# Kernel tuning notes

Hardware: AMD Instinct MI355X
Metric: run time of the kernel (lower is better)

The kernel has to match this reference:

```python
import jax, jax.numpy as jnp
import numpy as np

N = 768; H = 12; SQK = 16; SV = 16; PQK = 4; PV = 8; C = 384; PD = 128
EPS = 1e-8


def setup_inputs() -> dict:
    key = jax.random.key(0)
    ks = jax.random.split(key, 12)
    rn = lambda k, s, sc=1.0: jax.random.normal(k, s, jnp.float32) * sc
    return {
        'inputs_1d': rn(ks[0], (N, C)),
        'inputs_2d': rn(ks[1], (N, N, PD)),
        'mask': jnp.ones((N, 1), jnp.float32),
        'rotation': rn(ks[2], (9, N)),
        'translation': rn(ks[3], (3, N)),
        'wq': rn(ks[4], (C, H * SQK), C ** -0.5), 'bq': jnp.zeros((H * SQK,), jnp.float32),
        'wkv': rn(ks[5], (C, H * (SQK + SV)), C ** -0.5), 'bkv': jnp.zeros((H * (SQK + SV),), jnp.float32),
        'wqp': rn(ks[6], (C, H * 3 * PQK), C ** -0.5), 'bqp': jnp.zeros((H * 3 * PQK,), jnp.float32),
        'wkvp': rn(ks[7], (C, H * 3 * (PQK + PV)), C ** -0.5), 'bkvp': jnp.zeros((H * 3 * (PQK + PV),), jnp.float32),
        'tpw': jnp.ones((H,), jnp.float32),
        'w2d': rn(ks[8], (PD, H), PD ** -0.5), 'b2d': jnp.zeros((H,), jnp.float32),
        'wout': rn(ks[9], (H * (SV + 4 * PV + PD), C), 0.02), 'bout': jnp.zeros((C,), jnp.float32),
    }


def reference(inputs_1d, inputs_2d, mask, rotation, translation, wq, bq, wkv, bkv,
              wqp, bqp, wkvp, bkvp, tpw, w2d, b2d, wout, bout):
    n = inputs_1d.shape[0]
    R = rotation[:, :, None]
    T = translation[:, :, None]

    def apply_pt(x, y, z):  # global = R @ local + t, per residue
        return (R[0] * x + R[1] * y + R[2] * z + T[0],
                R[3] * x + R[4] * y + R[5] * z + T[1],
                R[6] * x + R[7] * y + R[8] * z + T[2])

    # scalar q/k/v
    qs = (inputs_1d @ wq + bq).reshape(n, H, SQK)
    kvs = (inputs_1d @ wkv + bkv).reshape(n, H, SQK + SV)
    ks_, vs = kvs[..., :SQK], kvs[..., SQK:]

    # point q and k/v in global frame
    qx, qy, qz = jnp.split(inputs_1d @ wqp + bqp, 3, axis=-1)
    q_pt = jnp.stack(apply_pt(qx, qy, qz), 0).reshape(3, n, H, PQK).transpose(0, 2, 1, 3)  # [3,H,N,PQK]
    kx, ky, kz = jnp.split(inputs_1d @ wkvp + bkvp, 3, axis=-1)
    kv_pt = jnp.stack(apply_pt(kx, ky, kz), 0).reshape(3, n, H, PQK + PV).transpose(0, 2, 1, 3)
    k_pt, v_pt = kv_pt[..., :PQK], kv_pt[..., PQK:]  # [3,H,N,PQK], [3,H,N,PV]

    # point attention term
    pw = jnp.sqrt(1.0 / (3 * 18)) * jax.nn.softplus(tpw)  # [H]
    dist2 = jnp.sum(jnp.square(q_pt[:, :, :, None, :] - k_pt[:, :, None, :, :]), axis=0)  # [H,N,N,PQK]
    attn_qk_point = -0.5 * jnp.sum(pw[:, None, None, None] * dist2, axis=-1)  # [H,N,N]

    # scalar attention term
    sw = jnp.sqrt(1.0 / (3 * 16))
    attn_qk_scalar = jnp.einsum('ihc,jhc->hij', sw * qs, ks_)

    # pair bias
    att2d = jnp.sqrt(1.0 / 3) * jnp.transpose(inputs_2d @ w2d + b2d, (2, 0, 1))  # [H,N,N]

    mask2d = mask * mask.T  # [N,N]
    logits = attn_qk_scalar + attn_qk_point + att2d - 50.0 * (1.0 - mask2d)
    attn = jax.nn.softmax(logits, axis=-1)  # [H,N,N]

    # weighted values
    res_scalar = jnp.einsum('hij,jhc->ihc', attn, vs).reshape(n, H * SV)
    res_pt = jnp.einsum('hij,dhjp->dihp', attn, v_pt).reshape(3, n, H * PV)

    # invert rigid: local = R^T @ (global - t)
    gx, gy, gz = res_pt[0] - T[0], res_pt[1] - T[1], res_pt[2] - T[2]
    lx = R[0] * gx + R[3] * gy + R[6] * gz
    ly = R[1] * gx + R[4] * gy + R[7] * gz
    lz = R[2] * gx + R[5] * gy + R[8] * gz
    dist = jnp.sqrt(EPS + lx * lx + ly * ly + lz * lz)

    res2d = jnp.einsum('hij,ijc->ihc', attn, inputs_2d).reshape(n, H * PD)

    feat = jnp.concatenate([res_scalar, lx, ly, lz, dist, res2d], axis=-1)  # [N, 2112]
    return feat @ wout + bout
```

## Files before the change

kernel.cpp:

```cpp
#include <hip/hip_runtime.h>
#include <cstdint>
#include <cstddef>


#define N_RES 768
#define NHEAD 12
#define NN (768*768)

__device__ __forceinline__ float softplusf_(float x) {
  return (x > 20.f) ? x : log1pf(__expf(x));
}

__global__ __launch_bounds__(256) void pack_b_kernel(
    const float* __restrict__ wq, const float* __restrict__ wkv,
    const float* __restrict__ wqp, const float* __restrict__ wkvp,
    float* __restrict__ B_all)
{
  int idx4 = blockIdx.x * 256 + threadIdx.x;
  int k = idx4 / 288;
  int n = (idx4 - k*288) * 4;
  float4 v;
  if (n < 192)       v = *(const float4*)(wq   + (size_t)k*192 + n);
  else if (n < 576)  v = *(const float4*)(wkv  + (size_t)k*384 + (n-192));
  else if (n < 720)  v = *(const float4*)(wqp  + (size_t)k*144 + (n-576));
  else               v = *(const float4*)(wkvp + (size_t)k*432 + (n-720));
  *(float4*)(B_all + (size_t)k*1152 + n) = v;
}

__global__ __launch_bounds__(256) void pack_small_kernel(
    const float* __restrict__ bq, const float* __restrict__ bkv,
    const float* __restrict__ bqp, const float* __restrict__ bkvp,
    const float* __restrict__ w2d,
    float* __restrict__ bias_all, float* __restrict__ wT)
{
  int idx = blockIdx.x * 256 + threadIdx.x;
  if (idx < 1152) {
    float v;
    if (idx < 192)      v = bq[idx];
    else if (idx < 576) v = bkv[idx-192];
    else if (idx < 720) v = bqp[idx-576];
    else                v = bkvp[idx-720];
    bias_all[idx] = v;
  } else if (idx < 2688) {
    int t = idx - 1152;
    int h = t >> 7, c = t & 127;
    wT[h*128 + c] = 0.5773502691896258f * w2d[c*12 + h];
  }
}

__global__ __launch_bounds__(256) void gemm_kernel(
    const float* __restrict__ A, int lda,
    const float* __restrict__ B, int ldb,
    const float* __restrict__ bias,
    float* __restrict__ C, int ldc,
    int M, int K, int kPerSplit)
{
  __shared__ float As[16][68];
  __shared__ float Bs[16][68];
  const int tid = threadIdx.x;
  const int m0 = blockIdx.y * 64, n0 = blockIdx.x * 64;
  const int kbeg = blockIdx.z * kPerSplit;
  const int kend = kbeg + kPerSplit;
  const int tn = tid & 15, tm = tid >> 4;
  float acc[4][4] = {};
  for (int k0 = kbeg; k0 < kend; k0 += 16) {
    {
      int idx = tid * 4;
      int m = idx >> 4, kk = idx & 15;
      float4 a = *(const float4*)(A + (size_t)(m0+m)*lda + k0 + kk);
      As[kk+0][m] = a.x; As[kk+1][m] = a.y; As[kk+2][m] = a.z; As[kk+3][m] = a.w;
    }
    {
      int kk = tid >> 4, n = (tid & 15) * 4;
      float4 b = *(const float4*)(B + (size_t)(k0+kk)*ldb + n0 + n);
      *(float4*)&Bs[kk][n] = b;
    }
    __syncthreads();
    #pragma unroll
    for (int k = 0; k < 16; ++k) {
      float4 a = *(const float4*)&As[k][tm*4];
      float4 b = *(const float4*)&Bs[k][tn*4];
      acc[0][0]=fmaf(a.x,b.x,acc[0][0]); acc[0][1]=fmaf(a.x,b.y,acc[0][1]);
      acc[0][2]=fmaf(a.x,b.z,acc[0][2]); acc[0][3]=fmaf(a.x,b.w,acc[0][3]);
      acc[1][0]=fmaf(a.y,b.x,acc[1][0]); acc[1][1]=fmaf(a.y,b.y,acc[1][1]);
      acc[1][2]=fmaf(a.y,b.z,acc[1][2]); acc[1][3]=fmaf(a.y,b.w,acc[1][3]);
      acc[2][0]=fmaf(a.z,b.x,acc[2][0]); acc[2][1]=fmaf(a.z,b.y,acc[2][1]);
      acc[2][2]=fmaf(a.z,b.z,acc[2][2]); acc[2][3]=fmaf(a.z,b.w,acc[2][3]);
      acc[3][0]=fmaf(a.w,b.x,acc[3][0]); acc[3][1]=fmaf(a.w,b.y,acc[3][1]);
      acc[3][2]=fmaf(a.w,b.z,acc[3][2]); acc[3][3]=fmaf(a.w,b.w,acc[3][3]);
    }
    __syncthreads();
  }
  float* Cp = C + (size_t)blockIdx.z * M * ldc;
  if (gridDim.z == 1) {
    #pragma unroll
    for (int r = 0; r < 4; ++r) {
      float* cp = Cp + (size_t)(m0 + tm*4 + r)*ldc + n0 + tn*4;
      #pragma unroll
      for (int c = 0; c < 4; ++c) cp[c] = acc[r][c] + bias[n0 + tn*4 + c];
    }
  } else {
    #pragma unroll
    for (int r = 0; r < 4; ++r) {
      float* cp = Cp + (size_t)(m0 + tm*4 + r)*ldc + n0 + tn*4;
      #pragma unroll
      for (int c = 0; c < 4; ++c) cp[c] = acc[r][c];
    }
  }
}

__global__ __launch_bounds__(256) void reduce_out_kernel(
    const float* __restrict__ part, const float* __restrict__ bout,
    float* __restrict__ out)
{
  int idx4 = blockIdx.x * 256 + threadIdx.x;
  if (idx4 >= 73728) return;
  int n4 = idx4 % 96;
  float4 a = *(const float4*)(bout + n4*4);
  #pragma unroll
  for (int z = 0; z < 6; ++z) {
    float4 p = *(const float4*)(part + (size_t)z*294912 + (size_t)idx4*4);
    a.x += p.x; a.y += p.y; a.z += p.z; a.w += p.w;
  }
  *(float4*)(out + (size_t)idx4*4) = a;
}

__global__ __launch_bounds__(256) void point_pack_kernel(
    const float* __restrict__ proj, const float* __restrict__ rot,
    const float* __restrict__ tra, const float* __restrict__ tpw,
    const float* __restrict__ b2d, const float* __restrict__ mask,
    float* __restrict__ Upack, float* __restrict__ Kpack, float* __restrict__ Vpack)
{
  int idx = blockIdx.x * 256 + threadIdx.x;
  if (idx >= N_RES * NHEAD) return;
  int i = idx / NHEAD, h = idx - i*NHEAD;
  float R[9], T[3];
  #pragma unroll
  for (int r = 0; r < 9; ++r) R[r] = rot[r*N_RES + i];
  #pragma unroll
  for (int d = 0; d < 3; ++d) T[d] = tra[d*N_RES + i];
  const float pw = 0.13608276348795434f * softplusf_(tpw[h]);
  const float sw = 0.14433756729740643f;
  const float s3 = 0.5773502691896258f;
  const float* prow = proj + (size_t)i * 1152;
  float* U  = Upack + ((size_t)h * N_RES + i) * 32;
  float* Kp = Kpack + ((size_t)h * N_RES + i) * 32;
  float* Vp = Vpack + (size_t)idx * 40;
  #pragma unroll
  for (int c = 0; c < 16; ++c) U[c]  = sw * prow[h*16 + c];
  #pragma unroll
  for (int c = 0; c < 16; ++c) Kp[c] = prow[192 + h*32 + c];
  #pragma unroll
  for (int c = 0; c < 16; ++c) Vp[c] = prow[192 + h*32 + 16 + c];
  float qn = 0.f;
  #pragma unroll
  for (int p = 0; p < 4; ++p) {
    float x = prow[576      + h*4 + p];
    float y = prow[576 + 48 + h*4 + p];
    float z = prow[576 + 96 + h*4 + p];
    #pragma unroll
    for (int d = 0; d < 3; ++d) {
      float v = R[3*d]*x + R[3*d+1]*y + R[3*d+2]*z + T[d];
      U[16 + d*4 + p] = pw * v;
      qn += v*v;
    }
  }
  float kn = 0.f;
  #pragma unroll
  for (int m = 0; m < 12; ++m) {
    float x = prow[720       + h*12 + m];
    float y = prow[720 + 144 + h*12 + m];
    float z = prow[720 + 288 + h*12 + m];
    #pragma unroll
    for (int d = 0; d < 3; ++d) {
      float v = R[3*d]*x + R[3*d+1]*y + R[3*d+2]*z + T[d];
      if (m < 4) { Kp[16 + d*4 + m] = v; kn += v*v; }
      else       { Vp[16 + d*8 + (m-4)] = v; }
    }
  }
  U[28] = -0.5f*pw*qn + s3*b2d[h] - 50.f;  U[29] = 50.f * mask[i];
  U[30] = -0.5f*pw;                        U[31] = 0.f;
  Kp[28] = 1.f;   Kp[29] = mask[i];
  Kp[30] = kn;    Kp[31] = 0.f;
}

__global__ __launch_bounds__(256) void logits_sp_kernel(
    const float* __restrict__ Upack, const float* __restrict__ Kpack,
    float* __restrict__ Lsp)
{
  __shared__ float Ut[64][33];
  __shared__ float Kt[64][33];
  const int h = blockIdx.z;
  const int i0 = blockIdx.y * 64, j0 = blockIdx.x * 64;
  const int tid = threadIdx.x;
  for (int t = tid; t < 512; t += 256) {
    int row = t >> 3, c4 = (t & 7) * 4;
    float4 u = *(const float4*)(Upack + ((size_t)h*N_RES + i0 + row)*32 + c4);
    float4 k = *(const float4*)(Kpack + ((size_t)h*N_RES + j0 + row)*32 + c4);
    Ut[row][c4+0]=u.x; Ut[row][c4+1]=u.y; Ut[row][c4+2]=u.z; Ut[row][c4+3]=u.w;
    Kt[row][c4+0]=k.x; Kt[row][c4+1]=k.y; Kt[row][c4+2]=k.z; Kt[row][c4+3]=k.w;
  }
  __syncthreads();
  const int tn = tid & 15, tm = tid >> 4;
  float acc[4][4] = {};
  #pragma unroll
  for (int k = 0; k < 32; ++k) {
    float a[4], b[4];
    #pragma unroll
    for (int r = 0; r < 4; ++r) a[r] = Ut[tm*4 + r][k];
    #pragma unroll
    for (int c = 0; c < 4; ++c) b[c] = Kt[tn*4 + c][k];
    #pragma unroll
    for (int r = 0; r < 4; ++r)
      #pragma unroll
      for (int c = 0; c < 4; ++c)
        acc[r][c] = fmaf(a[r], b[c], acc[r][c]);
  }
  #pragma unroll
  for (int r = 0; r < 4; ++r) {
    float4 v = make_float4(acc[r][0], acc[r][1], acc[r][2], acc[r][3]);
    *(float4*)(Lsp + (size_t)h*NN + (size_t)(i0 + tm*4 + r)*N_RES + j0 + tn*4) = v;
  }
}

__global__ __launch_bounds__(256) void fused_attn_kernel(
    const float* __restrict__ in2d, const float* __restrict__ wT,
    float* __restrict__ logits,
    float* __restrict__ invS, float* __restrict__ feat)
{
  __shared__ __align__(16) float Pt[128][12];
  __shared__ float comb[12][128];
  __shared__ float inv_sh[12];
  const int i = blockIdx.x;
  const int tid = threadIdx.x;
  const int wave = tid >> 6, lane = tid & 63;
  const int h0 = wave * 3;
  const int hu = __builtin_amdgcn_readfirstlane(h0);
  const float* w0 = wT + hu*128;
  float s_run[3] = {0.f, 0.f, 0.f};
  const int oc = tid & 127, ohalf = tid >> 7;
  float oacc[12];
  #pragma unroll
  for (int h = 0; h < 12; ++h) oacc[h] = 0.f;

  for (int jt = 0; jt < 6; ++jt) {
    const int j0 = jt * 128;
    #pragma unroll
    for (int half = 0; half < 2; ++half) {
      const int j = j0 + half*64 + lane;
      float l3[3];
      #pragma unroll
      for (int r = 0; r < 3; ++r)
        l3[r] = logits[(size_t)(h0+r)*NN + (size_t)i*N_RES + j];
      {
        const float* xrow = in2d + ((size_t)i*N_RES + j) * 128;
        float t0 = 0.f, t1 = 0.f, t2 = 0.f;
        #pragma unroll 8
        for (int c4 = 0; c4 < 32; ++c4) {
          float4 x  = *(const float4*)(xrow + c4*4);
          float4 wa = *(const float4*)(w0 + c4*4);
          float4 wb = *(const float4*)(w0 + 128 + c4*4);
          float4 wc = *(const float4*)(w0 + 256 + c4*4);
          t0 = fmaf(x.x,wa.x, fmaf(x.y,wa.y, fmaf(x.z,wa.z, fmaf(x.w,wa.w, t0))));
          t1 = fmaf(x.x,wb.x, fmaf(x.y,wb.y, fmaf(x.z,wb.z, fmaf(x.w,wb.w, t1))));
          t2 = fmaf(x.x,wc.x, fmaf(x.y,wc.y, fmaf(x.z,wc.z, fmaf(x.w,wc.w, t2))));
        }
        l3[0] += t0; l3[1] += t1; l3[2] += t2;
      }
      #pragma unroll
      for (int r = 0; r < 3; ++r) {
        logits[(size_t)(h0+r)*NN + (size_t)i*N_RES + j] = l3[r];
        float p = __expf(l3[r]);
        s_run[r] += p;
        Pt[half*64 + lane][h0 + r] = p;
      }
    }
    __syncthreads();
    {
      const float* xb = in2d + ((size_t)i*N_RES + j0 + ohalf*64) * 128 + oc;
      #pragma unroll 4
      for (int jj = 0; jj < 64; ++jj) {
        int row = ohalf*64 + jj;
        float x = xb[(size_t)jj * 128];
        float4 p0 = *(const float4*)&Pt[row][0];
        float4 p1 = *(const float4*)&Pt[row][4];
        float4 p2 = *(const float4*)&Pt[row][8];
        oacc[0] = fmaf(p0.x, x, oacc[0]);
        oacc[1] = fmaf(p0.y, x, oacc[1]);
        oacc[2] = fmaf(p0.z, x, oacc[2]);
        oacc[3] = fmaf(p0.w, x, oacc[3]);
        oacc[4] = fmaf(p1.x, x, oacc[4]);
        oacc[5] = fmaf(p1.y, x, oacc[5]);
        oacc[6] = fmaf(p1.z, x, oacc[6]);
        oacc[7] = fmaf(p1.w, x, oacc[7]);
        oacc[8] = fmaf(p2.x, x, oacc[8]);
        oacc[9] = fmaf(p2.y, x, oacc[9]);
        oacc[10] = fmaf(p2.z, x, oacc[10]);
        oacc[11] = fmaf(p2.w, x, oacc[11]);
      }
    }
    __syncthreads();
  }
  #pragma unroll
  for (int r = 0; r < 3; ++r) {
    float s = s_run[r];
    #pragma unroll
    for (int off = 32; off; off >>= 1) s += __shfl_xor(s, off);
    if (lane == 0) {
      float inv = 1.f / s;
      inv_sh[h0 + r] = inv;
      invS[(size_t)i*12 + h0 + r] = inv;
    }
  }
  if (ohalf == 1) {
    #pragma unroll
    for (int h = 0; h < 12; ++h) comb[h][oc] = oacc[h];
  }
  __syncthreads();
  if (ohalf == 0) {
    float* f = feat + (size_t)i*2112 + 576;
    #pragma unroll
    for (int h = 0; h < 12; ++h)
      f[h*128 + oc] = (oacc[h] + comb[h][oc]) * inv_sh[h];
  }
}

__global__ __launch_bounds__(256) void res_sv_pt_kernel(
    const float* __restrict__ logits, const float* __restrict__ invS,
    const float* __restrict__ Vpack, float* __restrict__ feat,
    float* __restrict__ rpt)
{
  __shared__ float at[16][132];
  __shared__ float vt[128][41];
  const int h = blockIdx.x;
  const int i0 = blockIdx.y * 16;
  const int tid = threadIdx.x;
  const int tn = tid & 15, tm = tid >> 4;
  float acc[3] = {};
  for (int j0 = 0; j0 < 768; j0 += 128) {
    for (int t = tid; t < 16*32; t += 256) {
      int ii = t >> 5, jf = t & 31;
      float4 v = *(const float4*)(logits + (size_t)h*NN + (size_t)(i0+ii)*N_RES + j0 + jf*4);
      float inv = invS[(size_t)(i0+ii)*12 + h];
      at[ii][jf*4+0] = __expf(v.x) * inv;
      at[ii][jf*4+1] = __expf(v.y) * inv;
      at[ii][jf*4+2] = __expf(v.z) * inv;
      at[ii][jf*4+3] = __expf(v.w) * inv;
    }
    for (int t = tid; t < 128*40; t += 256) {
      int jj = t / 40, c = t - jj*40;
      vt[jj][c] = Vpack[((size_t)(j0+jj)*12 + h)*40 + c];
    }
    __syncthreads();
    #pragma unroll 4
    for (int jj = 0; jj < 128; ++jj) {
      float a0 = at[tm][jj];
      acc[0] = fmaf(a0, vt[jj][tn*3+0], acc[0]);
      acc[1] = fmaf(a0, vt[jj][tn*3+1], acc[1]);
      acc[2] = fmaf(a0, vt[jj][tn*3+2], acc[2]);
    }
    __syncthreads();
  }
  const int i = i0 + tm;
  #pragma unroll
  for (int c = 0; c < 3; ++c) {
    int col = tn*3 + c;
    if (col < 16)      feat[(size_t)i*2112 + h*16 + col] = acc[c];
    else if (col < 40) rpt[((size_t)i*NHEAD + h)*24 + (col-16)] = acc[c];
  }
}

__global__ __launch_bounds__(256) void pt_epilogue_kernel(
    const float* __restrict__ rpt,
    const float* __restrict__ rot, const float* __restrict__ tra,
    float* __restrict__ feat)
{
  int idx = blockIdx.x * 256 + threadIdx.x;
  if (idx >= N_RES * 96) return;
  int i = idx / 96, m = idx - i*96;
  int h = m >> 3, p = m & 7;
  const float* rp = rpt + ((size_t)i*NHEAD + h)*24 + p;
  float gx = rp[0]  - tra[i];
  float gy = rp[8]  - tra[N_RES + i];
  float gz = rp[16] - tra[2*N_RES + i];
  float lx = rot[0*N_RES+i]*gx + rot[3*N_RES+i]*gy + rot[6*N_RES+i]*gz;
  float ly = rot[1*N_RES+i]*gx + rot[4*N_RES+i]*gy + rot[7*N_RES+i]*gz;
  float lz = rot[2*N_RES+i]*gx + rot[5*N_RES+i]*gy + rot[8*N_RES+i]*gz;
  float dist = sqrtf(1e-8f + lx*lx + ly*ly + lz*lz);
  float* f = feat + (size_t)i*2112 + 192;
  f[m]       = lx;
  f[96 + m]  = ly;
  f[192 + m] = lz;
  f[288 + m] = dist;
}

extern "C" void kernel_launch(void* const* d_in, const int* in_sizes, int n_in,
                              void* d_out, int out_size, void* d_ws, size_t ws_size,
                              hipStream_t stream)
{
  const float* in1d = (const float*)d_in[0];
  const float* in2d = (const float*)d_in[1];
  const float* mask = (const float*)d_in[2];
  const float* rot  = (const float*)d_in[3];
  const float* tra  = (const float*)d_in[4];
  const float* wq   = (const float*)d_in[5];
  const float* bq   = (const float*)d_in[6];
  const float* wkv  = (const float*)d_in[7];
  const float* bkv  = (const float*)d_in[8];
  const float* wqp  = (const float*)d_in[9];
  const float* bqp  = (const float*)d_in[10];
  const float* wkvp = (const float*)d_in[11];
  const float* bkvp = (const float*)d_in[12];
  const float* tpw  = (const float*)d_in[13];
  const float* w2d  = (const float*)d_in[14];
  const float* b2d  = (const float*)d_in[15];
  const float* wout = (const float*)d_in[16];
  const float* bout = (const float*)d_in[17];
  float* out = (float*)d_out;

  float* ws = (float*)d_ws;
  float* Upack    = ws;
  float* Kpack    = ws + 294912;
  float* Vpack    = ws + 589824;
  float* wT       = ws + 958464;
  float* feat     = ws + 960000;
  float* invS     = ws + 2582016;
  float* rpt      = ws + 2591232;
  float* proj_all = ws + 2812416;
  float* B_all    = ws + 3697152;
  float* bias_all = ws + 4139520;
  float* logits   = ws + 2812416;
  float* part     = ws + 2812416;

  pack_b_kernel<<<432, 256, 0, stream>>>(wq, wkv, wqp, wkvp, B_all);
  pack_small_kernel<<<11, 256, 0, stream>>>(bq, bkv, bqp, bkvp, w2d, bias_all, wT);
  gemm_kernel<<<dim3(18,12,1), 256, 0, stream>>>(in1d, 384, B_all, 1152, bias_all,
                                                 proj_all, 1152, 768, 384, 384);
  point_pack_kernel<<<36, 256, 0, stream>>>(proj_all, rot, tra, tpw, b2d, mask,
                                            Upack, Kpack, Vpack);
  logits_sp_kernel<<<dim3(12,12,12), 256, 0, stream>>>(Upack, Kpack, logits);
  fused_attn_kernel<<<N_RES, 256, 0, stream>>>(in2d, wT, logits, invS, feat);
  res_sv_pt_kernel<<<dim3(12,48), 256, 0, stream>>>(logits, invS, Vpack, feat, rpt);
  pt_epilogue_kernel<<<288, 256, 0, stream>>>(rpt, rot, tra, feat);
  gemm_kernel<<<dim3(6,12,6), 256, 0, stream>>>(feat, 2112, wout, 384, nullptr,
                                                part, 384, 768, 2112, 352);
  reduce_out_kernel<<<288, 256, 0, stream>>>(part, bout, out);
}
```

Baseline: 306.5 us.

## Split fused attention over key halves with atomic accumulation and finalize pass

The fused pair-bias/softmax/res2d kernel now splits each query row's 768 keys into two blocks of 384, doubling the grid. Each block atomically adds its partial softmax denominators and unnormalized res2d sums into zeroed global accumulators. A new finalize kernel then computes the inverse sums and writes the normalized res2d features. The aim is more concurrent waves to hide latency while streaming the large 2D input. The cost is an extra zeroing kernel, a finalize launch, atomic traffic and more workspace.

```diff
diff --git a/kernel.cpp b/kernel.cpp
--- a/kernel.cpp
+++ b/kernel.cpp
@@ -46,6 +46,11 @@
     int h = t >> 7, c = t & 127;
     wT[h*128 + c] = 0.5773502691896258f * w2d[c*12 + h];
   }
+}
+
+__global__ __launch_bounds__(256) void zero_kernel(float4* __restrict__ p)
+{
+  p[(size_t)blockIdx.x * 256 + threadIdx.x] = make_float4(0.f, 0.f, 0.f, 0.f);
 }
 
 __global__ __launch_bounds__(256) void gemm_kernel(
@@ -226,12 +231,11 @@
 __global__ __launch_bounds__(256) void fused_attn_kernel(
     const float* __restrict__ in2d, const float* __restrict__ wT,
     float* __restrict__ logits,
-    float* __restrict__ invS, float* __restrict__ feat)
+    float* __restrict__ res2dacc, float* __restrict__ psumacc)
 {
   __shared__ __align__(16) float Pt[128][12];
   __shared__ float comb[12][128];
-  __shared__ float inv_sh[12];
-  const int i = blockIdx.x;
+  const int i = blockIdx.y, z = blockIdx.x;
   const int tid = threadIdx.x;
   const int wave = tid >> 6, lane = tid & 63;
   const int h0 = wave * 3;
@@ -243,8 +247,8 @@
   #pragma unroll
   for (int h = 0; h < 12; ++h) oacc[h] = 0.f;
 
-  for (int jt = 0; jt < 6; ++jt) {
-    const int j0 = jt * 128;
+  for (int jt = 0; jt < 3; ++jt) {
+    const int j0 = z*384 + jt*128;
     #pragma unroll
     for (int half = 0; half < 2; ++half) {
       const int j = j0 + half*64 + lane;
@@ -306,11 +310,7 @@
     float s = s_run[r];
     #pragma unroll
     for (int off = 32; off; off >>= 1) s += __shfl_xor(s, off);
-    if (lane == 0) {
-      float inv = 1.f / s;
-      inv_sh[h0 + r] = inv;
-      invS[(size_t)i*12 + h0 + r] = inv;
-    }
+    if (lane == 0) atomicAdd(&psumacc[(size_t)i*12 + h0 + r], s);
   }
   if (ohalf == 1) {
     #pragma unroll
@@ -318,10 +318,31 @@
   }
   __syncthreads();
   if (ohalf == 0) {
-    float* f = feat + (size_t)i*2112 + 576;
+    float* pr = res2dacc + (size_t)i*1536;
     #pragma unroll
     for (int h = 0; h < 12; ++h)
-      f[h*128 + oc] = (oacc[h] + comb[h][oc]) * inv_sh[h];
+      atomicAdd(&pr[h*128 + oc], oacc[h] + comb[h][oc]);
+  }
+}
+
+__global__ __launch_bounds__(256) void finalize_kernel(
+    const float* __restrict__ res2dacc, const float* __restrict__ psumacc,
+    float* __restrict__ invS, float* __restrict__ feat)
+{
+  __shared__ float inv_sh[12];
+  const int i = blockIdx.x;
+  const int tid = threadIdx.x;
+  if (tid < 12) {
+    float inv = 1.f / psumacc[(size_t)i*12 + tid];
+    inv_sh[tid] = inv;
+    invS[(size_t)i*12 + tid] = inv;
+  }
+  __syncthreads();
+  #pragma unroll
+  for (int k = 0; k < 6; ++k) {
+    int idx = tid + k*256;
+    int h = idx >> 7;
+    feat[(size_t)i*2112 + 576 + idx] = res2dacc[(size_t)i*1536 + idx] * inv_sh[h];
   }
 }
 
@@ -426,20 +447,25 @@
   float* feat     = ws + 960000;
   float* invS     = ws + 2582016;
   float* rpt      = ws + 2591232;
-  float* proj_all = ws + 2812416;
-  float* B_all    = ws + 3697152;
-  float* bias_all = ws + 4139520;
-  float* logits   = ws + 2812416;
-  float* part     = ws + 2812416;
+  float* res2dacc = ws + 2812416;
+  float* psumacc  = ws + 3992064;
+  float* proj_all = ws + 4001280;
+  float* B_all    = ws + 4886016;
+  float* bias_all = ws + 5328384;
+  float* logits   = ws + 4001280;
+  float* part     = ws + 4001280;
 
   pack_b_kernel<<<432, 256, 0, stream>>>(wq, wkv, wqp, wkvp, B_all);
   pack_small_kernel<<<11, 256, 0, stream>>>(bq, bkv, bqp, bkvp, w2d, bias_all, wT);
+  zero_kernel<<<1161, 256, 0, stream>>>((float4*)res2dacc);
   gemm_kernel<<<dim3(18,12,1), 256, 0, stream>>>(in1d, 384, B_all, 1152, bias_all,
                                                  proj_all, 1152, 768, 384, 384);
   point_pack_kernel<<<36, 256, 0, stream>>>(proj_all, rot, tra, tpw, b2d, mask,
                                             Upack, Kpack, Vpack);
   logits_sp_kernel<<<dim3(12,12,12), 256, 0, stream>>>(Upack, Kpack, logits);
-  fused_attn_kernel<<<N_RES, 256, 0, stream>>>(in2d, wT, logits, invS, feat);
+  fused_attn_kernel<<<dim3(2, N_RES), 256, 0, stream>>>(
+      in2d, wT, logits, res2dacc, psumacc);
+  finalize_kernel<<<N_RES, 256, 0, stream>>>(res2dacc, psumacc, invS, feat);
   res_sv_pt_kernel<<<dim3(12,48), 256, 0, stream>>>(logits, invS, Vpack, feat, rpt);
   pt_epilogue_kernel<<<288, 256, 0, stream>>>(rpt, rot, tra, feat);
   gemm_kernel<<<dim3(6,12,6), 256, 0, stream>>>(feat, 2112, wout, 384, nullptr,
```

New measurement: 314.7 us. +2.7%, slower.
